# Kernel tuning notes

Hardware: AMD Instinct MI355X
Metric: run time of the kernel (lower is better)

Reference implementation:

```python
import jax, jax.numpy as jnp
import numpy as np

EPS = 1e-5

def _conv1x1(x, w, b):
    # x: (b,c,t,h,w), w: (o,c), b: (o,)  -> (b,o,t,h,w)
    return jnp.einsum('bcthw,oc->bothw', x, w) + b[None, :, None, None, None]

def setup_inputs() -> dict:
    key = jax.random.key(0)
    ks = jax.random.split(key, 12)
    B, C, IC, T, H, W = 32, 1024, 512, 8, 16, 8
    s_c = 1.0 / np.sqrt(C)
    s_ic = 1.0 / np.sqrt(IC)
    return {
        'x':       jax.random.normal(ks[0], (B, C, T, H, W), jnp.float32),
        'g_w':     jax.random.normal(ks[1], (IC, C), jnp.float32) * s_c,
        'g_b':     jax.random.normal(ks[2], (IC,), jnp.float32) * 0.01,
        'theta_w': jax.random.normal(ks[3], (IC, C), jnp.float32) * s_c,
        'theta_b': jax.random.normal(ks[4], (IC,), jnp.float32) * 0.01,
        'phi_w':   jax.random.normal(ks[5], (IC, C), jnp.float32) * s_c,
        'phi_b':   jax.random.normal(ks[6], (IC,), jnp.float32) * 0.01,
        'w_w':     jax.random.normal(ks[7], (C, IC), jnp.float32) * s_ic,
        'w_b':     jax.random.normal(ks[8], (C,), jnp.float32) * 0.01,
        'bn_gamma': jax.random.normal(ks[9], (C,), jnp.float32) * 0.1 + 1.0,
        'bn_beta':  jax.random.normal(ks[10], (C,), jnp.float32) * 0.01,
        'bn_mean':  jax.random.normal(ks[11], (C,), jnp.float32) * 0.01,
        'bn_var':   jnp.ones((C,), jnp.float32),
    }

def reference(x, g_w, g_b, theta_w, theta_b, phi_w, phi_b, w_w, w_b,
              bn_gamma, bn_beta, bn_mean, bn_var):
    B, C, T, H, W = x.shape
    IC = g_w.shape[0]
    # value projection, flattened per frame: (b, t, ic*h*w)
    g_x = _conv1x1(x, g_w, g_b)                       # (b,ic,t,h,w)
    g_x = jnp.transpose(g_x, (0, 2, 1, 3, 4)).reshape(B, T, IC * H * W)
    # pooled query/key over spatial dims: (b,t,ic) and (b,ic,t)
    theta = _conv1x1(x, theta_w, theta_b).mean(axis=(3, 4))   # (b,ic,t)
    phi = _conv1x1(x, phi_w, phi_b).mean(axis=(3, 4))         # (b,ic,t)
    f = jnp.einsum('bct,bcs->bts', theta, phi)                # (b,t,t)
    attn = jax.nn.softmax(f, axis=-1)
    y = jnp.einsum('bts,bsd->btd', attn, g_x)                 # (b,t,ic*h*w)
    y = jnp.transpose(y.reshape(B, T, IC, H, W), (0, 2, 1, 3, 4))  # (b,ic,t,h,w)
    # output projection + BatchNorm3d (inference stats) + residual
    wy = _conv1x1(y, w_w, w_b)                        # (b,c,t,h,w)
    inv = bn_gamma / jnp.sqrt(bn_var + EPS)
    wy = wy * inv[None, :, None, None, None] + (bn_beta - bn_mean * inv)[None, :, None, None, None]
    return wy + x
```

## Files before the change

kernel.cpp:

```cpp
#include <hip/hip_runtime.h>
#include <hip/hip_bf16.h>

typedef __attribute__((ext_vector_type(8))) short bf16x8;
typedef __attribute__((ext_vector_type(4))) float f32x4;

__global__ __launch_bounds__(256) void pool_kernel(const float* __restrict__ x,
                                                   float* __restrict__ xbar) {
    int row = blockIdx.x * 16 + (threadIdx.x >> 4);
    int j = threadIdx.x & 15;
    const float4* p = (const float4*)(x + (size_t)row * 128);
    float4 a = p[j * 2], b2 = p[j * 2 + 1];
    float s = a.x + a.y + a.z + a.w + b2.x + b2.y + b2.z + b2.w;
    s += __shfl_xor(s, 1); s += __shfl_xor(s, 2);
    s += __shfl_xor(s, 4); s += __shfl_xor(s, 8);
    if (j == 0) xbar[row] = s * (1.0f / 128.0f);
}

__global__ __launch_bounds__(256) void thetaphi_kernel(
        const float* __restrict__ xbar,
        const float* __restrict__ tw, const float* __restrict__ tb,
        const float* __restrict__ pw, const float* __restrict__ pb,
        float* __restrict__ theta, float* __restrict__ phi) {
    int which = blockIdx.x & 1;
    int icc = (blockIdx.x >> 1) & 15;
    int b = blockIdx.x >> 5;
    const float* w = which ? pw : tw;
    const float* bias = which ? pb : tb;
    float* out = which ? phi : theta;
    __shared__ float xs[8192];
    for (int i = threadIdx.x; i < 8192; i += 256) xs[i] = xbar[b * 8192 + i];
    __syncthreads();
    int icl = threadIdx.x >> 3;
    int t = threadIdx.x & 7;
    int ic = icc * 32 + icl;
    const float* wr = w + (size_t)ic * 1024;
    float acc = 0.0f;
    #pragma unroll 8
    for (int k = 0; k < 1024; k++) acc += wr[k] * xs[k * 8 + t];
    out[((size_t)b * 512 + ic) * 8 + t] = acc + bias[ic];
}

__global__ __launch_bounds__(64) void attn_kernel(const float* __restrict__ theta,
                                                  const float* __restrict__ phi,
                                                  float* __restrict__ attn) {
    __shared__ float th[4096], ph[4096];
    int b = blockIdx.x, lane = threadIdx.x;
    for (int i = lane; i < 4096; i += 64) {
        th[i] = theta[(size_t)b * 4096 + i];
        ph[i] = phi[(size_t)b * 4096 + i];
    }
    __syncthreads();
    int t = lane >> 3, s = lane & 7;
    float f = 0.0f;
    #pragma unroll 8
    for (int ic = 0; ic < 512; ic++) f += th[ic * 8 + t] * ph[ic * 8 + s];
    float m = f;
    m = fmaxf(m, __shfl_xor(m, 1));
    m = fmaxf(m, __shfl_xor(m, 2));
    m = fmaxf(m, __shfl_xor(m, 4));
    float e = __expf(f - m);
    float sum = e;
    sum += __shfl_xor(sum, 1); sum += __shfl_xor(sum, 2); sum += __shfl_xor(sum, 4);
    attn[b * 64 + lane] = e / sum;
}

__global__ __launch_bounds__(256) void prep_operands_kernel(
        const float* __restrict__ gw, const float* __restrict__ ww,
        __hip_bfloat16* __restrict__ gwt, __hip_bfloat16* __restrict__ wwb) {
    int bid = blockIdx.x;
    if (bid < 512) {
        int icb = bid >> 5;
        int cb = bid & 31;
        __shared__ float tile[32][33];
        int r = threadIdx.x >> 5, c = threadIdx.x & 31;
        #pragma unroll
        for (int i = 0; i < 4; i++)
            tile[r + i * 8][c] = gw[(size_t)(icb * 32 + r + i * 8) * 1024 + cb * 32 + c];
        __syncthreads();
        #pragma unroll
        for (int i = 0; i < 4; i++) {
            int cin = cb * 32 + r + i * 8;
            gwt[(size_t)cin * 512 + icb * 32 + c] = __float2bfloat16(tile[c][r + i * 8]);
        }
    } else {
        int b2 = bid - 512;
        size_t base = (size_t)b2 * 2048 + (size_t)threadIdx.x * 8;
        const float4* src = (const float4*)(ww + base);
        float4 v0 = src[0], v1 = src[1];
        __hip_bfloat16 tmp[8];
        tmp[0] = __float2bfloat16(v0.x); tmp[1] = __float2bfloat16(v0.y);
        tmp[2] = __float2bfloat16(v0.z); tmp[3] = __float2bfloat16(v0.w);
        tmp[4] = __float2bfloat16(v1.x); tmp[5] = __float2bfloat16(v1.y);
        tmp[6] = __float2bfloat16(v1.z); tmp[7] = __float2bfloat16(v1.w);
        *(bf16x8*)(wwb + base) = *(const bf16x8*)tmp;
    }
}

#if defined(__has_builtin)
#if __has_builtin(__builtin_amdgcn_global_load_lds)
#define USE_GLOAD_LDS 1
#endif
#endif

__device__ __forceinline__ void gload_lds16(const void* g, void* ldsbase) {
#ifdef USE_GLOAD_LDS
    __builtin_amdgcn_global_load_lds(
        (__attribute__((address_space(1))) void*)(g),
        (__attribute__((address_space(3))) void*)(ldsbase), 16, 0, 0);
#endif
}

__global__ __launch_bounds__(256) void prepM_mfma_kernel(
        const __hip_bfloat16* __restrict__ wwb,
        const __hip_bfloat16* __restrict__ gwt,
        __hip_bfloat16* __restrict__ M) {
    __shared__ __align__(16) __hip_bfloat16 As[128 * 32];
    __shared__ __align__(16) __hip_bfloat16 Bs[128 * 32];
    int bid = blockIdx.x;
    int mb = bid >> 3, nb = bid & 7;
    int c0 = mb * 128, n0 = nb * 128;
    int tid = threadIdx.x;
    int w = tid >> 6, l = tid & 63;
    int wr = w >> 1, wc = w & 1;
    const __hip_bfloat16* Ab = wwb + (size_t)c0 * 512;
    const __hip_bfloat16* Bb = gwt + (size_t)n0 * 512;
    int arow = tid >> 2, akq = tid & 3;
    f32x4 acc[4][4] = {};

    for (int kk = 0; kk < 16; ++kk) {
        int k0 = kk * 32;
#ifdef USE_GLOAD_LDS
        gload_lds16(Ab + (size_t)arow * 512 + k0 + akq * 8,        (char*)As + w * 1024);
        gload_lds16(Ab + (size_t)(arow + 64) * 512 + k0 + akq * 8, (char*)As + 4096 + w * 1024);
        gload_lds16(Bb + (size_t)arow * 512 + k0 + akq * 8,        (char*)Bs + w * 1024);
        gload_lds16(Bb + (size_t)(arow + 64) * 512 + k0 + akq * 8, (char*)Bs + 4096 + w * 1024);
#else
        *(bf16x8*)((char*)As + (size_t)tid * 16)        = *(const bf16x8*)(Ab + (size_t)arow * 512 + k0 + akq * 8);
        *(bf16x8*)((char*)As + 4096 + (size_t)tid * 16) = *(const bf16x8*)(Ab + (size_t)(arow + 64) * 512 + k0 + akq * 8);
        *(bf16x8*)((char*)Bs + (size_t)tid * 16)        = *(const bf16x8*)(Bb + (size_t)arow * 512 + k0 + akq * 8);
        *(bf16x8*)((char*)Bs + 4096 + (size_t)tid * 16) = *(const bf16x8*)(Bb + (size_t)(arow + 64) * 512 + k0 + akq * 8);
#endif
        __syncthreads();
        const __hip_bfloat16* Ap = As + ((size_t)(wr * 64 + (l & 15)) * 32) + (l >> 4) * 8;
        const __hip_bfloat16* Bp = Bs + ((size_t)(wc * 64 + (l & 15)) * 32) + (l >> 4) * 8;
        bf16x8 af[4], bfr[4];
        #pragma unroll
        for (int m = 0; m < 4; m++) af[m] = *(const bf16x8*)(Ap + m * 16 * 32);
        #pragma unroll
        for (int n = 0; n < 4; n++) bfr[n] = *(const bf16x8*)(Bp + n * 16 * 32);
        #pragma unroll
        for (int m = 0; m < 4; m++)
            #pragma unroll
            for (int n = 0; n < 4; n++)
                acc[m][n] = __builtin_amdgcn_mfma_f32_16x16x32_bf16(af[m], bfr[n], acc[m][n], 0, 0, 0);
        __syncthreads();
    }

    int col = l & 15, rg = l >> 4;
    #pragma unroll
    for (int m = 0; m < 4; m++)
        #pragma unroll
        for (int j = 0; j < 4; j++) {
            int gc = c0 + wr * 64 + m * 16 + rg * 4 + j;
            #pragma unroll
            for (int n = 0; n < 4; n++)
                M[(size_t)gc * 1024 + n0 + wc * 64 + n * 16 + col] = __float2bfloat16(acc[m][n][j]);
        }
}

__global__ __launch_bounds__(256) void prepbias_kernel(
        const float* __restrict__ ww, const float* __restrict__ gb,
        const float* __restrict__ wb, const float* __restrict__ gamma,
        const float* __restrict__ beta, const float* __restrict__ mean,
        const float* __restrict__ var, float* __restrict__ inv,
        float* __restrict__ shift) {
    int wv = threadIdx.x >> 6, l = threadIdx.x & 63;
    int c = blockIdx.x * 32 + wv * 8 + (l >> 3);
    int j = l & 7;
    const float* wr = ww + (size_t)c * 512;
    float acc = 0.0f;
    #pragma unroll 8
    for (int k = j; k < 512; k += 8) acc += wr[k] * gb[k];
    acc += __shfl_xor(acc, 1); acc += __shfl_xor(acc, 2); acc += __shfl_xor(acc, 4);
    if (j == 0) {
        float cb = wb[c] + acc;
        float iv = gamma[c] * rsqrtf(var[c] + 1e-5f);
        inv[c] = iv;
        shift[c] = cb * iv + beta[c] - mean[c] * iv;
    }
}

__global__ __launch_bounds__(256) void mix_kernel(const float* __restrict__ x,
                                                  const float* __restrict__ attn,
                                                  __hip_bfloat16* __restrict__ xmt) {
    int orig = blockIdx.x;
    int wg = (orig & 7) * 64 + (orig >> 3);
    int b = wg >> 4;
    int hwg = wg & 15;
    __shared__ float at[64];
    __shared__ float xs[8][8][33];
    int tid = threadIdx.x;
    if (tid < 64) at[tid] = attn[b * 64 + tid];
    int ci = tid >> 3, s = tid & 7;
    int h = tid >> 5, cq = tid & 31;
    const float* xb = x + ((size_t)b << 20);
    __hip_bfloat16* ob = xmt + ((size_t)b << 20);
    for (int cc = 0; cc < 32; ++cc) {
        const float4* src = (const float4*)(xb + ((size_t)(cc * 32 + ci) * 8 + s) * 128 + hwg * 8);
        float4 v0 = src[0], v1 = src[1];
        __syncthreads();
        xs[s][0][ci] = v0.x; xs[s][1][ci] = v0.y; xs[s][2][ci] = v0.z; xs[s][3][ci] = v0.w;
        xs[s][4][ci] = v1.x; xs[s][5][ci] = v1.y; xs[s][6][ci] = v1.z; xs[s][7][ci] = v1.w;
        __syncthreads();
        float xr[8];
        #pragma unroll
        for (int ss = 0; ss < 8; ss++) xr[ss] = xs[ss][h][cq];
        #pragma unroll
        for (int t = 0; t < 8; t++) {
            float o = 0.0f;
            #pragma unroll
            for (int ss = 0; ss < 8; ss++) o += at[t * 8 + ss] * xr[ss];
            ob[(size_t)(t * 128 + hwg * 8 + h) * 1024 + cc * 32 + cq] = __float2bfloat16(o);
        }
    }
}

__global__ __launch_bounds__(512, 2) void gemm256_kernel(
        const __hip_bfloat16* __restrict__ Mw,
        const __hip_bfloat16* __restrict__ xmt,
        const float* __restrict__ x,
        const float* __restrict__ inv, const float* __restrict__ shift,
        float* __restrict__ out) {
    __shared__ __align__(16) __hip_bfloat16 As[2][256 * 64];
    __shared__ __align__(16) __hip_bfloat16 Bs[2][256 * 64];
    const int TSZ = 256 * 64 * 2;

    int orig = blockIdx.x;
    int bid = (orig & 7) * 64 + (orig >> 3);
    int b = bid >> 4;
    int mb = (bid >> 2) & 3;
    int nb = bid & 3;
    int c0 = mb * 256, n0 = nb * 256;

    int tid = threadIdx.x;
    int w = tid >> 6, l = tid & 63;
    int wr = w >> 2, wc = w & 3;

    int srow = l >> 3;
    int xcol = (l & 7) ^ srow;
    const __hip_bfloat16* aSrc = Mw + (size_t)(c0 + w * 32 + srow) * 1024 + xcol * 8;
    const __hip_bfloat16* bSrc = xmt + ((size_t)b << 20) + (size_t)(n0 + w * 32 + srow) * 1024 + xcol * 8;
    int stBase = w * 4096;

    int xs_ = (l & 7) << 4;
    int cb = (l >> 4) << 4;
    int x0 = cb ^ xs_;
    int x1 = (64 | cb) ^ xs_;
    int aRow128 = (wr * 128 + (l & 15)) * 128;
    int bRow128 = (wc * 64 + (l & 15)) * 128;

    char* AsB = (char*)As;
    char* BsB = (char*)Bs;
    f32x4 acc[8][4] = {};

    #define STAGE_PH(nbuf, ph) do {                                                   \
        gload_lds16(aSrc + (ph) * 8192, AsB + (nbuf) * TSZ + stBase + (ph) * 1024);   \
        gload_lds16(bSrc + (ph) * 8192, BsB + (nbuf) * TSZ + stBase + (ph) * 1024);   \
    } while (0)

    #define TILE(curb, PREF) do {                                                     \
        _Pragma("unroll")                                                             \
        for (int ks = 0; ks < 2; ++ks) {                                              \
            int xk = ks ? x1 : x0;                                                    \
            bf16x8 bfr[4];                                                            \
            _Pragma("unroll")                                                         \
            for (int n = 0; n < 4; ++n)                                               \
                bfr[n] = *(const bf16x8*)(BsB + (curb) * TSZ + bRow128 + n * 2048 + xk); \
            _Pragma("unroll")                                                         \
            for (int mh = 0; mh < 2; ++mh) {                                          \
                bf16x8 af[4];                                                         \
                _Pragma("unroll")                                                     \
                for (int mi = 0; mi < 4; ++mi)                                        \
                    af[mi] = *(const bf16x8*)(AsB + (curb) * TSZ + aRow128 + (mh * 4 + mi) * 2048 + xk); \
                if (PREF) STAGE_PH((curb) ^ 1, ks * 2 + mh);                          \
                __builtin_amdgcn_s_setprio(1);                                        \
                _Pragma("unroll")                                                     \
                for (int mi = 0; mi < 4; ++mi)                                        \
                    _Pragma("unroll")                                                 \
                    for (int n = 0; n < 4; ++n)                                       \
                        acc[mh * 4 + mi][n] = __builtin_amdgcn_mfma_f32_16x16x32_bf16( \
                            af[mi], bfr[n], acc[mh * 4 + mi][n], 0, 0, 0);            \
                __builtin_amdgcn_s_setprio(0);                                        \
            }                                                                         \
        }                                                                             \
    } while (0)

    #define SYNC_ADV() do {                                                           \
        aSrc += 64; bSrc += 64;                                                       \
        asm volatile("s_waitcnt vmcnt(0)" ::: "memory");                              \
        __builtin_amdgcn_s_barrier();                                                 \
        __builtin_amdgcn_sched_barrier(0);                                            \
    } while (0)

    #pragma unroll
    for (int ph = 0; ph < 4; ++ph) STAGE_PH(0, ph);
    SYNC_ADV();

    #pragma unroll 1
    for (int t = 0; t < 7; ++t) {
        TILE(0, 1); SYNC_ADV();
        TILE(1, 1); SYNC_ADV();
    }
    TILE(0, 1); SYNC_ADV();
    TILE(1, 0);

    #undef STAGE_PH
    #undef TILE
    #undef SYNC_ADV

    int col = l & 15, rg = l >> 4;
    const float* xb = x + ((size_t)b << 20);
    float* ob = out + ((size_t)b << 20);
    #pragma unroll
    for (int mi = 0; mi < 8; ++mi) {
        #pragma unroll
        for (int j = 0; j < 4; ++j) {
            int gc = c0 + wr * 128 + mi * 16 + rg * 4 + j;
            float iv = inv[gc], sh = shift[gc];
            size_t rowoff = (size_t)gc * 1024 + n0 + wc * 64 + col;
            #pragma unroll
            for (int n = 0; n < 4; ++n) {
                size_t idx = rowoff + n * 16;
                ob[idx] = acc[mi][n][j] * iv + sh + xb[idx];
            }
        }
    }
}

extern "C" void kernel_launch(void* const* d_in, const int* in_sizes, int n_in,
                              void* d_out, int out_size, void* d_ws, size_t ws_size,
                              hipStream_t stream) {
    const float* x    = (const float*)d_in[0];
    const float* g_w  = (const float*)d_in[1];
    const float* g_b  = (const float*)d_in[2];
    const float* th_w = (const float*)d_in[3];
    const float* th_b = (const float*)d_in[4];
    const float* ph_w = (const float*)d_in[5];
    const float* ph_b = (const float*)d_in[6];
    const float* w_w  = (const float*)d_in[7];
    const float* w_b  = (const float*)d_in[8];
    const float* gam  = (const float*)d_in[9];
    const float* bet  = (const float*)d_in[10];
    const float* mea  = (const float*)d_in[11];
    const float* var  = (const float*)d_in[12];
    float* out = (float*)d_out;
    char* ws = (char*)d_ws;

    __hip_bfloat16* xmt = (__hip_bfloat16*)ws;
    __hip_bfloat16* Mw  = (__hip_bfloat16*)(ws + 67108864);
    float* xbar  = (float*)(ws + 69206016);
    float* theta = (float*)(ws + 70254592);
    float* phi   = (float*)(ws + 70778880);
    float* attn  = (float*)(ws + 71303168);
    float* inv   = (float*)(ws + 71311360);
    float* shift = (float*)(ws + 71315456);
    __hip_bfloat16* gwt = (__hip_bfloat16*)ws;
    __hip_bfloat16* wwb = (__hip_bfloat16*)(ws + 1048576);

    hipLaunchKernelGGL(pool_kernel, dim3(16384), dim3(256), 0, stream, x, xbar);
    hipLaunchKernelGGL(thetaphi_kernel, dim3(1024), dim3(256), 0, stream,
                       xbar, th_w, th_b, ph_w, ph_b, theta, phi);
    hipLaunchKernelGGL(attn_kernel, dim3(32), dim3(64), 0, stream, theta, phi, attn);
    hipLaunchKernelGGL(prep_operands_kernel, dim3(768), dim3(256), 0, stream,
                       g_w, w_w, gwt, wwb);
    hipLaunchKernelGGL(prepM_mfma_kernel, dim3(64), dim3(256), 0, stream, wwb, gwt, Mw);
    hipLaunchKernelGGL(prepbias_kernel, dim3(32), dim3(256), 0, stream,
                       w_w, g_b, w_b, gam, bet, mea, var, inv, shift);
    hipLaunchKernelGGL(mix_kernel, dim3(512), dim3(256), 0, stream, x, attn, xmt);
    hipLaunchKernelGGL(gemm256_kernel, dim3(512), dim3(512), 0, stream,
                       Mw, xmt, x, inv, shift, out);
}
```

Baseline: 248.8 us.

## Use four-stage K=32 LDS ring with partial vmcnt waits in final GEMM

The output-projection GEMM moves from a double buffer with K=64 tiles to a four-slot ring of K=32 tiles. Loads run three stages ahead, and each step waits only until older loads finish (vmcnt(8)) rather than draining all loads. The LDS swizzle and read addressing are rewritten for the 64-byte row layout. The aim is to hide global-to-LDS latency behind MFMA work, at the cost of twice as many barriers and shorter compute per step.

```diff
diff --git a/kernel.cpp b/kernel.cpp
--- a/kernel.cpp
+++ b/kernel.cpp
@@ -231,9 +231,9 @@
         const float* __restrict__ x,
         const float* __restrict__ inv, const float* __restrict__ shift,
         float* __restrict__ out) {
-    __shared__ __align__(16) __hip_bfloat16 As[2][256 * 64];
-    __shared__ __align__(16) __hip_bfloat16 Bs[2][256 * 64];
-    const int TSZ = 256 * 64 * 2;
+    __shared__ __align__(16) __hip_bfloat16 HBs[65536];
+    char* AH = (char*)HBs;
+    const int BUFB = 32768;
 
     int orig = blockIdx.x;
     int bid = (orig & 7) * 64 + (orig >> 3);
@@ -246,77 +246,75 @@
     int w = tid >> 6, l = tid & 63;
     int wr = w >> 2, wc = w & 3;
 
-    int srow = l >> 3;
-    int xcol = (l & 7) ^ srow;
-    const __hip_bfloat16* aSrc = Mw + (size_t)(c0 + w * 32 + srow) * 1024 + xcol * 8;
-    const __hip_bfloat16* bSrc = xmt + ((size_t)b << 20) + (size_t)(n0 + w * 32 + srow) * 1024 + xcol * 8;
-    int stBase = w * 4096;
-
-    int xs_ = (l & 7) << 4;
-    int cb = (l >> 4) << 4;
-    int x0 = cb ^ xs_;
-    int x1 = (64 | cb) ^ xs_;
-    int aRow128 = (wr * 128 + (l & 15)) * 128;
-    int bRow128 = (wc * 64 + (l & 15)) * 128;
-
-    char* AsB = (char*)As;
-    char* BsB = (char*)Bs;
+    int sgl = (((l & 3) - ((l >> 3) & 3)) & 3);
+    const __hip_bfloat16* aS = Mw + (size_t)(c0 + w * 16 + (l >> 2)) * 1024 + sgl * 8;
+    const __hip_bfloat16* bS = xmt + ((size_t)b << 20) + (size_t)(n0 + w * 16 + (l >> 2)) * 1024 + sgl * 8;
+    int stBase = w * 1024;
+
+    int rdSlot = ((l >> 4) + (((l & 15) >> 1) & 3)) & 3;
+    int aRdBase = (wr * 128 + (l & 15)) * 64 + rdSlot * 16;
+    int bRdBase = 16384 + (wc * 64 + (l & 15)) * 64 + rdSlot * 16;
+
     f32x4 acc[8][4] = {};
 
-    #define STAGE_PH(nbuf, ph) do {                                                   \
-        gload_lds16(aSrc + (ph) * 8192, AsB + (nbuf) * TSZ + stBase + (ph) * 1024);   \
-        gload_lds16(bSrc + (ph) * 8192, BsB + (nbuf) * TSZ + stBase + (ph) * 1024);   \
+    #define ISSUE(q3) do {                                                      \
+        gload_lds16(aS,              AH + (q3) * BUFB + stBase);                \
+        gload_lds16(aS + 128 * 1024, AH + (q3) * BUFB + stBase + 8192);         \
+        gload_lds16(bS,              AH + (q3) * BUFB + 16384 + stBase);        \
+        gload_lds16(bS + 128 * 1024, AH + (q3) * BUFB + 16384 + stBase + 8192); \
+        aS += 32; bS += 32;                                                     \
     } while (0)
 
-    #define TILE(curb, PREF) do {                                                     \
-        _Pragma("unroll")                                                             \
-        for (int ks = 0; ks < 2; ++ks) {                                              \
-            int xk = ks ? x1 : x0;                                                    \
-            bf16x8 bfr[4];                                                            \
-            _Pragma("unroll")                                                         \
-            for (int n = 0; n < 4; ++n)                                               \
-                bfr[n] = *(const bf16x8*)(BsB + (curb) * TSZ + bRow128 + n * 2048 + xk); \
-            _Pragma("unroll")                                                         \
-            for (int mh = 0; mh < 2; ++mh) {                                          \
-                bf16x8 af[4];                                                         \
-                _Pragma("unroll")                                                     \
-                for (int mi = 0; mi < 4; ++mi)                                        \
-                    af[mi] = *(const bf16x8*)(AsB + (curb) * TSZ + aRow128 + (mh * 4 + mi) * 2048 + xk); \
-                if (PREF) STAGE_PH((curb) ^ 1, ks * 2 + mh);                          \
-                __builtin_amdgcn_s_setprio(1);                                        \
-                _Pragma("unroll")                                                     \
-                for (int mi = 0; mi < 4; ++mi)                                        \
-                    _Pragma("unroll")                                                 \
-                    for (int n = 0; n < 4; ++n)                                       \
-                        acc[mh * 4 + mi][n] = __builtin_amdgcn_mfma_f32_16x16x32_bf16( \
-                            af[mi], bfr[n], acc[mh * 4 + mi][n], 0, 0, 0);            \
-                __builtin_amdgcn_s_setprio(0);                                        \
-            }                                                                         \
-        }                                                                             \
+    #define V8 asm volatile("s_waitcnt vmcnt(8)" ::: "memory")
+    #define V4 asm volatile("s_waitcnt vmcnt(4)" ::: "memory")
+    #define V0 asm volatile("s_waitcnt vmcnt(0)" ::: "memory")
+
+    #define HSTEP(q, DOISS, WAITM, LAST) do {                                   \
+        if (DOISS) ISSUE(((q) + 3) & 3);                                        \
+        const char* bufA = AH + (q) * BUFB;                                     \
+        bf16x8 bfr[4];                                                          \
+        _Pragma("unroll")                                                       \
+        for (int n = 0; n < 4; ++n)                                             \
+            bfr[n] = *(const bf16x8*)(bufA + bRdBase + n * 1024);               \
+        __builtin_amdgcn_s_setprio(1);                                          \
+        _Pragma("unroll")                                                       \
+        for (int mi = 0; mi < 8; ++mi) {                                        \
+            bf16x8 af = *(const bf16x8*)(bufA + aRdBase + mi * 1024);           \
+            _Pragma("unroll")                                                   \
+            for (int n = 0; n < 4; ++n)                                         \
+                acc[mi][n] = __builtin_amdgcn_mfma_f32_16x16x32_bf16(           \
+                    af, bfr[n], acc[mi][n], 0, 0, 0);                           \
+        }                                                                       \
+        __builtin_amdgcn_s_setprio(0);                                          \
+        if (!LAST) {                                                            \
+            WAITM;                                                              \
+            __builtin_amdgcn_s_barrier();                                       \
+            __builtin_amdgcn_sched_barrier(0);                                  \
+        }                                                                       \
     } while (0)
 
-    #define SYNC_ADV() do {                                                           \
-        aSrc += 64; bSrc += 64;                                                       \
-        asm volatile("s_waitcnt vmcnt(0)" ::: "memory");                              \
-        __builtin_amdgcn_s_barrier();                                                 \
-        __builtin_amdgcn_sched_barrier(0);                                            \
-    } while (0)
-
-    #pragma unroll
-    for (int ph = 0; ph < 4; ++ph) STAGE_PH(0, ph);
-    SYNC_ADV();
+    ISSUE(0); ISSUE(1); ISSUE(2);
+    V8;
+    __builtin_amdgcn_s_barrier();
+    __builtin_amdgcn_sched_barrier(0);
 
     #pragma unroll 1
     for (int t = 0; t < 7; ++t) {
-        TILE(0, 1); SYNC_ADV();
-        TILE(1, 1); SYNC_ADV();
-    }
-    TILE(0, 1); SYNC_ADV();
-    TILE(1, 0);
-
-    #undef STAGE_PH
-    #undef TILE
-    #undef SYNC_ADV
+        HSTEP(0, 1, V8, 0);
+        HSTEP(1, 1, V8, 0);
+        HSTEP(2, 1, V8, 0);
+        HSTEP(3, 1, V8, 0);
+    }
+    HSTEP(0, 1, V8, 0);
+    HSTEP(1, 0, V4, 0);
+    HSTEP(2, 0, V0, 0);
+    HSTEP(3, 0, V0, 1);
+
+    #undef ISSUE
+    #undef HSTEP
+    #undef V8
+    #undef V4
+    #undef V0
 
     int col = l & 15, rg = l >> 4;
     const float* xb = x + ((size_t)b << 20);
```

After: 238.2 us. -4.2%, faster.
